# Kernel optimization log

Hardware: AMD Instinct MI355X
Metric: run time of the kernel (lower is better)

## Reference

```python
import jax, jax.numpy as jnp
import numpy as np

NUM_CLASSES = 10
ALPHA = 0.25
GAMMA = 2.0
BETA = 1.0
EPS = 1e-7


def _corners(centers, dims, yaws):
    # centers [N,2], dims [N,2] (l,w), yaws [N] -> corners [N,4,2]
    half = dims * 0.5
    base = jnp.array([[1., 1.], [-1., 1.], [-1., -1.], [1., -1.]], dtype=centers.dtype)
    base = base[None, :, :] * half[:, None, :]  # [N,4,2]
    c, s = jnp.cos(yaws), jnp.sin(yaws)
    x = base[..., 0] * c[:, None] - base[..., 1] * s[:, None]
    y = base[..., 0] * s[:, None] + base[..., 1] * c[:, None]
    corners = jnp.stack([x, y], axis=-1) + centers[:, None, :]
    return corners[:, jnp.array([3, 2, 1, 0]), :]  # reorder as in torch code


def _cross(u, v):
    return u[..., 0] * v[..., 1] - u[..., 1] * v[..., 0]


def _signed_area(q):  # q [...,4,2]
    return 0.5 * jnp.sum(_cross(q, jnp.roll(q, -1, axis=-2)), axis=-1)


def _pts_in_quad(pts, quad, sgn):
    # pts [N,P,2] inside convex quad [N,4,2]; sgn = orientation sign of quad [N]
    a = quad
    e = jnp.roll(quad, -1, axis=-2) - a  # [N,4,2]
    d = pts[:, :, None, :] - a[:, None, :, :]  # [N,P,4,2]
    cr = e[:, None, :, 0] * d[..., 1] - e[:, None, :, 1] * d[..., 0]  # [N,P,4]
    return jnp.all(cr * sgn[:, None, None] >= -1e-9, axis=-1)


def _rotated_iou(cA, cB):
    # Exact convex-quad intersection IoU (replaces the per-box Shapely loop).
    N = cA.shape[0]
    sgnA = jnp.sign(_signed_area(cA))
    sgnB = jnp.sign(_signed_area(cB))
    vA_in_B = _pts_in_quad(cA, cB, sgnB)  # [N,4]
    vB_in_A = _pts_in_quad(cB, cA, sgnA)  # [N,4]
    # all 4x4 edge-edge intersections
    a1 = cA; a2 = jnp.roll(cA, -1, axis=1)
    b1 = cB; b2 = jnp.roll(cB, -1, axis=1)
    da = (a2 - a1)[:, :, None, :]  # [N,4,1,2]
    db = (b2 - b1)[:, None, :, :]  # [N,1,4,2]
    dp = b1[:, None, :, :] - a1[:, :, None, :]  # [N,4,4,2]
    den = _cross(da, db)  # [N,4,4]
    den_safe = jnp.where(jnp.abs(den) < 1e-12, 1.0, den)
    t = _cross(dp, db) / den_safe
    s = _cross(dp, da) / den_safe
    val_x = (jnp.abs(den) > 1e-12) & (t >= 0) & (t <= 1) & (s >= 0) & (s <= 1)
    xpts = a1[:, :, None, :] + t[..., None] * da  # [N,4,4,2]
    # up to 24 candidate vertices of the convex intersection polygon
    pts = jnp.concatenate([cA, cB, xpts.reshape(N, 16, 2)], axis=1)  # [N,24,2]
    valid = jnp.concatenate([vA_in_B, vB_in_A, val_x.reshape(N, 16)], axis=1)
    pts = jnp.where(valid[..., None], pts, 0.0)
    nv = valid.sum(axis=1)
    cent = pts.sum(axis=1) / jnp.maximum(nv, 1)[:, None]
    ang = jnp.arctan2(pts[..., 1] - cent[:, None, 1], pts[..., 0] - cent[:, None, 0])
    key = jnp.where(valid, ang, 1e9)
    order = jnp.argsort(key, axis=1)
    ps = jnp.take_along_axis(pts, order[..., None], axis=1)
    vs = jnp.take_along_axis(valid, order, axis=1)
    ps = jnp.where(vs[..., None], ps, ps[:, :1, :])  # pad with first valid vertex
    inter = 0.5 * jnp.abs(jnp.sum(_cross(ps, jnp.roll(ps, -1, axis=1)), axis=1))
    inter = jnp.where(nv >= 3, inter, 0.0)
    areaA = jnp.abs(_signed_area(cA))
    areaB = jnp.abs(_signed_area(cB))
    union = areaA + areaB - inter
    return jnp.where(union > 1e-7, inter / union, 0.0)


def _sl1(p, t):
    d = jnp.abs(p - t)
    return jnp.where(d < BETA, 0.5 * d * d / BETA, d - 0.5 * BETA)


def setup_inputs() -> dict:
    key = jax.random.key(0)
    ks = jax.random.split(key, 7)
    B, C, H, W = 8, NUM_CLASSES, 256, 256
    cls_pred = jax.random.normal(ks[0], (B, C, H, W), dtype=jnp.float32)
    reg_pred = jax.random.uniform(ks[1], (B, 9, H, W), dtype=jnp.float32)
    iou_pred = jax.random.normal(ks[2], (B, 1, H, W), dtype=jnp.float32)
    cls_targets = jax.random.randint(ks[3], (B, H, W), 0, C, dtype=jnp.int32)
    reg_targets = jax.random.uniform(ks[4], (B, 9, H, W), dtype=jnp.float32)
    reg_weights = jax.random.randint(ks[5], (B, H, W), 0, 2).astype(jnp.float32)
    iou_targets = jax.random.uniform(ks[6], (B, 1, H, W), dtype=jnp.float32)
    return {"cls_pred": cls_pred, "reg_pred": reg_pred, "iou_pred": iou_pred,
            "cls_targets": cls_targets, "reg_targets": reg_targets,
            "reg_weights": reg_weights, "iou_targets": iou_targets}


def reference(cls_pred, reg_pred, iou_pred, cls_targets, reg_targets, reg_weights, iou_targets):
    B, C, H, W = cls_pred.shape
    N = B * H * W
    clsf = jnp.transpose(cls_pred, (0, 2, 3, 1)).reshape(N, C)
    regf = jnp.transpose(reg_pred, (0, 2, 3, 1)).reshape(N, 9)
    regt = jnp.transpose(reg_targets, (0, 2, 3, 1)).reshape(N, 9)
    iouf = jnp.transpose(iou_pred, (0, 2, 3, 1)).reshape(N)
    iout = iou_targets.reshape(N)
    ct = cls_targets.reshape(N)
    w = reg_weights.reshape(N)
    pos = (w > 0).astype(clsf.dtype)
    num_pos = jnp.maximum(pos.sum(), 1.0)
    # focal classification loss
    valid = ct >= 0
    p = jax.nn.softmax(clsf, axis=1)
    tl = jnp.clip(ct, 0, C - 1)
    pt = jnp.clip(jnp.take_along_axis(p, tl[:, None], axis=1)[:, 0], EPS, 1.0 - EPS)
    alpha_t = jnp.where(ct > 0, ALPHA, 1.0 - ALPHA)
    fl = -alpha_t * (1.0 - pt) ** GAMMA * jnp.log(pt)
    cls_loss = jnp.sum(jnp.where(valid, fl, 0.0)) / num_pos
    cen_p, dim_p, yaw_p = regf[:, :2], regf[:, 3:5], regf[:, 6]
    cen_t, dim_t, yaw_t = regt[:, :2], regt[:, 3:5], regt[:, 6]
    cp = _corners(cen_p, dim_p, yaw_p)
    ctg = _corners(cen_t, dim_t, yaw_t)
    iou = jax.lax.stop_gradient(_rotated_iou(cp, ctg))
    d2 = jnp.sum((cen_p - cen_t) ** 2, axis=-1)
    allc = jnp.concatenate([cp, ctg], axis=1)  # [N,8,2]
    c2 = jnp.maximum(jnp.sum((allc.max(axis=1) - allc.min(axis=1)) ** 2, axis=-1), EPS)
    loss_bev = 1.0 - iou + d2 / c2
    at_p = jnp.arctan(dim_p[:, 1] / jnp.maximum(dim_p[:, 0], EPS))
    at_t = jnp.arctan(dim_t[:, 1] / jnp.maximum(dim_t[:, 0], EPS))
    v = (4.0 / np.pi ** 2) * (at_p - at_t) ** 2
    alpha_c = jax.lax.stop_gradient(v / (1.0 - iou + v + EPS))
    loss_bev = loss_bev + alpha_c * v
    bev_loss = jnp.sum(loss_bev * pos) / num_pos
    # smooth-L1 terms: z (ch 2), h (ch 5), vel (ch 7:9)
    z_loss = jnp.sum(_sl1(regf[:, 2], regt[:, 2]) * pos) / num_pos
    h_loss = jnp.sum(_sl1(regf[:, 5], regt[:, 5]) * pos) / num_pos
    vel_loss = jnp.sum(_sl1(regf[:, 7:9], regt[:, 7:9]).sum(axis=-1) * pos) / num_pos
    # BCE-with-logits IoU head loss
    x, y = iouf, iout
    bce = jnp.maximum(x, 0.0) - x * y + jnp.log1p(jnp.exp(-jnp.abs(x)))
    iou_loss = jnp.sum(bce * pos) / num_pos
    return jnp.stack([cls_loss, bev_loss, z_loss, h_loss, vel_loss, iou_loss])
```

## Files before the change

kernel.cpp:

```cpp
#include <hip/hip_runtime.h>
#include <cstdint>
#include <cstddef>

#define B_ 8
#define C_ 10
#define HW_ 65536
#define NPIX_ (B_ * HW_)

__device__ __forceinline__ float sl1f(float p, float t) {
    float d = fabsf(p - t);
    return (d < 1.0f) ? 0.5f * d * d : d - 0.5f;
}

__device__ __forceinline__ void pixel_loss(
    const float lg[C_], int ct, const float P[9], const float T[9],
    float w, float xiou, float yiou, float o[7])
{
    float m = lg[0];
    #pragma unroll
    for (int c = 1; c < C_; c++) m = fmaxf(m, lg[c]);
    float se = 0.f;
    float ex[C_];
    #pragma unroll
    for (int c = 0; c < C_; c++) { ex[c] = __expf(lg[c] - m); se += ex[c]; }
    int tl = ct < 0 ? 0 : (ct > C_ - 1 ? C_ - 1 : ct);
    float et = 0.f;
    #pragma unroll
    for (int c = 0; c < C_; c++) et = (c == tl) ? ex[c] : et;
    float pt = __fdividef(et, se);
    pt = fminf(fmaxf(pt, 1e-7f), 1.0f - 1e-7f);
    float alpha_t = (ct > 0) ? 0.25f : 0.75f;
    float omp = 1.0f - pt;
    float fl = -alpha_t * omp * omp * __logf(pt);
    o[0] = (ct >= 0) ? fl : 0.0f;

    float pos = (w > 0.f) ? 1.f : 0.f;

    float Ax[4], Ay[4], Bx[4], By[4];
    {
        const float sbx[4] = { 1.f, -1.f, -1.f, 1.f };
        const float sby[4] = { -1.f, -1.f, 1.f, 1.f };
        float hx = 0.5f * P[3], hy = 0.5f * P[4];
        float ss, cc; __sincosf(P[6], &ss, &cc);
        #pragma unroll
        for (int i = 0; i < 4; i++) {
            float px = sbx[i] * hx, py = sby[i] * hy;
            Ax[i] = px * cc - py * ss + P[0];
            Ay[i] = px * ss + py * cc + P[1];
        }
        float hx2 = 0.5f * T[3], hy2 = 0.5f * T[4];
        float ss2, cc2; __sincosf(T[6], &ss2, &cc2);
        #pragma unroll
        for (int i = 0; i < 4; i++) {
            float px = sbx[i] * hx2, py = sby[i] * hy2;
            Bx[i] = px * cc2 - py * ss2 + T[0];
            By[i] = px * ss2 + py * cc2 + T[1];
        }
    }

    float sa = 0.f, sb = 0.f;
    #pragma unroll
    for (int i = 0; i < 4; i++) {
        int j = (i + 1) & 3;
        sa += Ax[i] * Ay[j] - Ay[i] * Ax[j];
        sb += Bx[i] * By[j] - By[i] * Bx[j];
    }
    sa *= 0.5f; sb *= 0.5f;
    float sgnA = (sa > 0.f) ? 1.f : ((sa < 0.f) ? -1.f : 0.f);
    float sgnB = (sb > 0.f) ? 1.f : ((sb < 0.f) ? -1.f : 0.f);

    float dB[4][4], dA[4][4];
    #pragma unroll
    for (int j = 0; j < 4; j++) {
        int j1 = (j + 1) & 3;
        float ex_ = Bx[j1] - Bx[j], ey_ = By[j1] - By[j];
        #pragma unroll
        for (int i = 0; i < 4; i++)
            dB[j][i] = sgnB * (ex_ * (Ay[i] - By[j]) - ey_ * (Ax[i] - Bx[j]));
    }
    #pragma unroll
    for (int j = 0; j < 4; j++) {
        int j1 = (j + 1) & 3;
        float ex_ = Ax[j1] - Ax[j], ey_ = Ay[j1] - Ay[j];
        #pragma unroll
        for (int i = 0; i < 4; i++)
            dA[j][i] = sgnA * (ex_ * (By[i] - Ay[j]) - ey_ * (Bx[i] - Ax[j]));
    }

    float S = 0.f;
    #pragma unroll
    for (int i = 0; i < 4; i++) {
        int i1 = (i + 1) & 3;
        float t0 = 0.f, t1 = 1.f;
        #pragma unroll
        for (int j = 0; j < 4; j++) {
            float d0 = dB[j][i], d1 = dB[j][i1];
            float den = d1 - d0;
            float t = __fdividef(-d0, den);
            if (den > 0.f)       t0 = fmaxf(t0, t);
            else if (den < 0.f)  t1 = fminf(t1, t);
            else if (d0 < 0.f)   t0 = 2.f;
        }
        S += (Ax[i] * Ay[i1] - Ay[i] * Ax[i1]) * fmaxf(t1 - t0, 0.f);
    }
    #pragma unroll
    for (int i = 0; i < 4; i++) {
        int i1 = (i + 1) & 3;
        float t0 = 0.f, t1 = 1.f;
        #pragma unroll
        for (int j = 0; j < 4; j++) {
            float d0 = dA[j][i], d1 = dA[j][i1];
            float den = d1 - d0;
            float t = __fdividef(-d0, den);
            if (den > 0.f)       t0 = fmaxf(t0, t);
            else if (den < 0.f)  t1 = fminf(t1, t);
            else if (d0 < 0.f)   t0 = 2.f;
        }
        S += (Bx[i] * By[i1] - By[i] * Bx[i1]) * fmaxf(t1 - t0, 0.f);
    }
    float inter = 0.5f * fabsf(S);

    float areaA = fabsf(sa), areaB = fabsf(sb);
    float uni = areaA + areaB - inter;
    float iou = (uni > 1e-7f) ? __fdividef(inter, uni) : 0.f;

    float ddx = P[0] - T[0], ddy = P[1] - T[1];
    float d2 = ddx * ddx + ddy * ddy;
    float mnx = Ax[0], mxx = Ax[0], mny = Ay[0], mxy = Ay[0];
    #pragma unroll
    for (int i = 1; i < 4; i++) {
        mnx = fminf(mnx, Ax[i]); mxx = fmaxf(mxx, Ax[i]);
        mny = fminf(mny, Ay[i]); mxy = fmaxf(mxy, Ay[i]);
    }
    #pragma unroll
    for (int i = 0; i < 4; i++) {
        mnx = fminf(mnx, Bx[i]); mxx = fmaxf(mxx, Bx[i]);
        mny = fminf(mny, By[i]); mxy = fmaxf(mxy, By[i]);
    }
    float exd = mxx - mnx, eyd = mxy - mny;
    float c2 = fmaxf(exd * exd + eyd * eyd, 1e-7f);

    float atp = atanf(__fdividef(P[4], fmaxf(P[3], 1e-7f)));
    float att = atanf(__fdividef(T[4], fmaxf(T[3], 1e-7f)));
    float dv = atp - att;
    float v = 0.4052847345693511f * dv * dv;
    float alpha_c = __fdividef(v, 1.0f - iou + v + 1e-7f);
    float lbev = 1.0f - iou + __fdividef(d2, c2) + alpha_c * v;
    o[1] = lbev * pos;

    o[2] = sl1f(P[2], T[2]) * pos;
    o[3] = sl1f(P[5], T[5]) * pos;
    o[4] = (sl1f(P[7], T[7]) + sl1f(P[8], T[8])) * pos;

    float bce = fmaxf(xiou, 0.f) - xiou * yiou + __logf(1.0f + __expf(-fabsf(xiou)));
    o[5] = bce * pos;
    o[6] = pos;
}

__global__ __launch_bounds__(256) void bev_loss_main(
    const float* __restrict__ cls_pred, const float* __restrict__ reg_pred,
    const float* __restrict__ iou_pred, const int* __restrict__ cls_tg,
    const float* __restrict__ reg_tg, const float* __restrict__ reg_w,
    const float* __restrict__ iou_tg, double* __restrict__ part)
{
    int t  = blockIdx.x * blockDim.x + threadIdx.x;
    int n0 = t << 1;
    int b  = n0 >> 16;
    int hw = n0 & 65535;

    float2 lg2[C_];
    {
        const float* cp = cls_pred + (size_t)b * C_ * HW_ + hw;
        #pragma unroll
        for (int c = 0; c < C_; c++)
            lg2[c] = *reinterpret_cast<const float2*>(cp + (size_t)c * HW_);
    }
    float2 P2[9], T2[9];
    {
        const float* rp = reg_pred + (size_t)b * 9 * HW_ + hw;
        const float* rt = reg_tg  + (size_t)b * 9 * HW_ + hw;
        #pragma unroll
        for (int k = 0; k < 9; k++) {
            P2[k] = *reinterpret_cast<const float2*>(rp + (size_t)k * HW_);
            T2[k] = *reinterpret_cast<const float2*>(rt + (size_t)k * HW_);
        }
    }
    int2   ct2 = *reinterpret_cast<const int2*>(cls_tg + n0);
    float2 w2  = *reinterpret_cast<const float2*>(reg_w + n0);
    float2 x2  = *reinterpret_cast<const float2*>(iou_pred + n0);
    float2 y2  = *reinterpret_cast<const float2*>(iou_tg + n0);

    float o0[7], o1[7];
    {
        float lg[C_], P[9], T[9];
        #pragma unroll
        for (int c = 0; c < C_; c++) lg[c] = lg2[c].x;
        #pragma unroll
        for (int k = 0; k < 9; k++) { P[k] = P2[k].x; T[k] = T2[k].x; }
        pixel_loss(lg, ct2.x, P, T, w2.x, x2.x, y2.x, o0);
    }
    {
        float lg[C_], P[9], T[9];
        #pragma unroll
        for (int c = 0; c < C_; c++) lg[c] = lg2[c].y;
        #pragma unroll
        for (int k = 0; k < 9; k++) { P[k] = P2[k].y; T[k] = T2[k].y; }
        pixel_loss(lg, ct2.y, P, T, w2.y, x2.y, y2.y, o1);
    }

    __shared__ double red[4][7];
    int lane = threadIdx.x & 63;
    int wv   = threadIdx.x >> 6;
    #pragma unroll
    for (int k = 0; k < 7; k++) {
        double s = (double)o0[k] + (double)o1[k];
        for (int off = 32; off > 0; off >>= 1) s += __shfl_down(s, off, 64);
        if (lane == 0) red[wv][k] = s;
    }
    __syncthreads();
    if (threadIdx.x == 0) {
        #pragma unroll
        for (int k = 0; k < 7; k++)
            part[(size_t)blockIdx.x * 7 + k] = red[0][k] + red[1][k] + red[2][k] + red[3][k];
    }
}

__global__ void bev_loss_fin(const double* __restrict__ part, float* __restrict__ out, int nb) {
    int l = threadIdx.x;
    double s[7] = { 0, 0, 0, 0, 0, 0, 0 };
    for (int i = l; i < nb; i += 64) {
        #pragma unroll
        for (int k = 0; k < 7; k++) s[k] += part[(size_t)i * 7 + k];
    }
    #pragma unroll
    for (int k = 0; k < 7; k++) {
        for (int off = 32; off > 0; off >>= 1) s[k] += __shfl_down(s[k], off, 64);
    }
    if (l == 0) {
        double npos = fmax(s[6], 1.0);
        #pragma unroll
        for (int k = 0; k < 6; k++) out[k] = (float)(s[k] / npos);
    }
}

extern "C" void kernel_launch(void* const* d_in, const int* in_sizes, int n_in,
                              void* d_out, int out_size, void* d_ws, size_t ws_size,
                              hipStream_t stream) {
    const float* cls_pred = (const float*)d_in[0];
    const float* reg_pred = (const float*)d_in[1];
    const float* iou_pred = (const float*)d_in[2];
    const int*   cls_tg   = (const int*)d_in[3];
    const float* reg_tg   = (const float*)d_in[4];
    const float* reg_w    = (const float*)d_in[5];
    const float* iou_tg   = (const float*)d_in[6];
    float* out = (float*)d_out;
    double* part = (double*)d_ws;

    const int nb = 1024;
    bev_loss_main<<<nb, 256, 0, stream>>>(cls_pred, reg_pred, iou_pred, cls_tg,
                                          reg_tg, reg_w, iou_tg, part);
    bev_loss_fin<<<1, 64, 0, stream>>>(part, out, nb);
}
```

Measured before the change: 37.77 us.

## Fuse final reduction into main kernel via atomic ticket and vectorize pixel math as float2

Replaces the separate finalize kernel with a last-block-done pattern: each block writes its partial sums, increments an atomic ticket, and the last block reduces all partials and writes the outputs. The per-pixel loss is rewritten to process two pixels as float2 lanes with branchless selects in the clipping loop, and launch bounds now request 3 waves per SIMD. It adds a memset launch for the ticket and a threadfence per block, trading the second kernel launch for extra synchronisation.

New measurement: 122.4 us. 3.24x slower.

```diff
diff --git a/kernel.cpp b/kernel.cpp
--- a/kernel.cpp
+++ b/kernel.cpp
@@ -6,240 +6,284 @@
 #define C_ 10
 #define HW_ 65536
 #define NPIX_ (B_ * HW_)
-
-__device__ __forceinline__ float sl1f(float p, float t) {
-    float d = fabsf(p - t);
-    return (d < 1.0f) ? 0.5f * d * d : d - 0.5f;
-}
-
-__device__ __forceinline__ void pixel_loss(
-    const float lg[C_], int ct, const float P[9], const float T[9],
-    float w, float xiou, float yiou, float o[7])
-{
-    float m = lg[0];
-    #pragma unroll
-    for (int c = 1; c < C_; c++) m = fmaxf(m, lg[c]);
-    float se = 0.f;
-    float ex[C_];
-    #pragma unroll
-    for (int c = 0; c < C_; c++) { ex[c] = __expf(lg[c] - m); se += ex[c]; }
-    int tl = ct < 0 ? 0 : (ct > C_ - 1 ? C_ - 1 : ct);
-    float et = 0.f;
-    #pragma unroll
-    for (int c = 0; c < C_; c++) et = (c == tl) ? ex[c] : et;
-    float pt = __fdividef(et, se);
-    pt = fminf(fmaxf(pt, 1e-7f), 1.0f - 1e-7f);
-    float alpha_t = (ct > 0) ? 0.25f : 0.75f;
-    float omp = 1.0f - pt;
-    float fl = -alpha_t * omp * omp * __logf(pt);
-    o[0] = (ct >= 0) ? fl : 0.0f;
-
-    float pos = (w > 0.f) ? 1.f : 0.f;
-
-    float Ax[4], Ay[4], Bx[4], By[4];
-    {
-        const float sbx[4] = { 1.f, -1.f, -1.f, 1.f };
-        const float sby[4] = { -1.f, -1.f, 1.f, 1.f };
-        float hx = 0.5f * P[3], hy = 0.5f * P[4];
-        float ss, cc; __sincosf(P[6], &ss, &cc);
-        #pragma unroll
-        for (int i = 0; i < 4; i++) {
-            float px = sbx[i] * hx, py = sby[i] * hy;
-            Ax[i] = px * cc - py * ss + P[0];
-            Ay[i] = px * ss + py * cc + P[1];
-        }
-        float hx2 = 0.5f * T[3], hy2 = 0.5f * T[4];
-        float ss2, cc2; __sincosf(T[6], &ss2, &cc2);
-        #pragma unroll
-        for (int i = 0; i < 4; i++) {
-            float px = sbx[i] * hx2, py = sby[i] * hy2;
-            Bx[i] = px * cc2 - py * ss2 + T[0];
-            By[i] = px * ss2 + py * cc2 + T[1];
-        }
-    }
-
-    float sa = 0.f, sb = 0.f;
-    #pragma unroll
-    for (int i = 0; i < 4; i++) {
-        int j = (i + 1) & 3;
-        sa += Ax[i] * Ay[j] - Ay[i] * Ax[j];
-        sb += Bx[i] * By[j] - By[i] * Bx[j];
-    }
-    sa *= 0.5f; sb *= 0.5f;
-    float sgnA = (sa > 0.f) ? 1.f : ((sa < 0.f) ? -1.f : 0.f);
-    float sgnB = (sb > 0.f) ? 1.f : ((sb < 0.f) ? -1.f : 0.f);
-
-    float dB[4][4], dA[4][4];
-    #pragma unroll
-    for (int j = 0; j < 4; j++) {
-        int j1 = (j + 1) & 3;
-        float ex_ = Bx[j1] - Bx[j], ey_ = By[j1] - By[j];
-        #pragma unroll
-        for (int i = 0; i < 4; i++)
-            dB[j][i] = sgnB * (ex_ * (Ay[i] - By[j]) - ey_ * (Ax[i] - Bx[j]));
-    }
-    #pragma unroll
-    for (int j = 0; j < 4; j++) {
-        int j1 = (j + 1) & 3;
-        float ex_ = Ax[j1] - Ax[j], ey_ = Ay[j1] - Ay[j];
-        #pragma unroll
-        for (int i = 0; i < 4; i++)
-            dA[j][i] = sgnA * (ex_ * (By[i] - Ay[j]) - ey_ * (Bx[i] - Ax[j]));
-    }
-
-    float S = 0.f;
-    #pragma unroll
-    for (int i = 0; i < 4; i++) {
-        int i1 = (i + 1) & 3;
-        float t0 = 0.f, t1 = 1.f;
-        #pragma unroll
-        for (int j = 0; j < 4; j++) {
-            float d0 = dB[j][i], d1 = dB[j][i1];
-            float den = d1 - d0;
-            float t = __fdividef(-d0, den);
-            if (den > 0.f)       t0 = fmaxf(t0, t);
-            else if (den < 0.f)  t1 = fminf(t1, t);
-            else if (d0 < 0.f)   t0 = 2.f;
-        }
-        S += (Ax[i] * Ay[i1] - Ay[i] * Ax[i1]) * fmaxf(t1 - t0, 0.f);
-    }
-    #pragma unroll
-    for (int i = 0; i < 4; i++) {
-        int i1 = (i + 1) & 3;
-        float t0 = 0.f, t1 = 1.f;
-        #pragma unroll
-        for (int j = 0; j < 4; j++) {
-            float d0 = dA[j][i], d1 = dA[j][i1];
-            float den = d1 - d0;
-            float t = __fdividef(-d0, den);
-            if (den > 0.f)       t0 = fmaxf(t0, t);
-            else if (den < 0.f)  t1 = fminf(t1, t);
-            else if (d0 < 0.f)   t0 = 2.f;
-        }
-        S += (Bx[i] * By[i1] - By[i] * Bx[i1]) * fmaxf(t1 - t0, 0.f);
-    }
-    float inter = 0.5f * fabsf(S);
-
-    float areaA = fabsf(sa), areaB = fabsf(sb);
-    float uni = areaA + areaB - inter;
-    float iou = (uni > 1e-7f) ? __fdividef(inter, uni) : 0.f;
-
-    float ddx = P[0] - T[0], ddy = P[1] - T[1];
-    float d2 = ddx * ddx + ddy * ddy;
-    float mnx = Ax[0], mxx = Ax[0], mny = Ay[0], mxy = Ay[0];
-    #pragma unroll
-    for (int i = 1; i < 4; i++) {
-        mnx = fminf(mnx, Ax[i]); mxx = fmaxf(mxx, Ax[i]);
-        mny = fminf(mny, Ay[i]); mxy = fmaxf(mxy, Ay[i]);
-    }
-    #pragma unroll
-    for (int i = 0; i < 4; i++) {
-        mnx = fminf(mnx, Bx[i]); mxx = fmaxf(mxx, Bx[i]);
-        mny = fminf(mny, By[i]); mxy = fmaxf(mxy, By[i]);
-    }
-    float exd = mxx - mnx, eyd = mxy - mny;
-    float c2 = fmaxf(exd * exd + eyd * eyd, 1e-7f);
-
-    float atp = atanf(__fdividef(P[4], fmaxf(P[3], 1e-7f)));
-    float att = atanf(__fdividef(T[4], fmaxf(T[3], 1e-7f)));
-    float dv = atp - att;
-    float v = 0.4052847345693511f * dv * dv;
-    float alpha_c = __fdividef(v, 1.0f - iou + v + 1e-7f);
-    float lbev = 1.0f - iou + __fdividef(d2, c2) + alpha_c * v;
-    o[1] = lbev * pos;
-
-    o[2] = sl1f(P[2], T[2]) * pos;
-    o[3] = sl1f(P[5], T[5]) * pos;
-    o[4] = (sl1f(P[7], T[7]) + sl1f(P[8], T[8])) * pos;
-
-    float bce = fmaxf(xiou, 0.f) - xiou * yiou + __logf(1.0f + __expf(-fabsf(xiou)));
-    o[5] = bce * pos;
-    o[6] = pos;
-}
-
-__global__ __launch_bounds__(256) void bev_loss_main(
+#define NB_ 1024
+
+__device__ __forceinline__ float2 mk2(float a, float b) { float2 r; r.x = a; r.y = b; return r; }
+__device__ __forceinline__ float2 bc2(float a) { return mk2(a, a); }
+__device__ __forceinline__ float2 add2(float2 a, float2 b) { return mk2(a.x + b.x, a.y + b.y); }
+__device__ __forceinline__ float2 sub2(float2 a, float2 b) { return mk2(a.x - b.x, a.y - b.y); }
+__device__ __forceinline__ float2 mul2(float2 a, float2 b) { return mk2(a.x * b.x, a.y * b.y); }
+__device__ __forceinline__ float2 fma2(float2 a, float2 b, float2 c) {
+    return mk2(fmaf(a.x, b.x, c.x), fmaf(a.y, b.y, c.y));
+}
+__device__ __forceinline__ float2 max2(float2 a, float2 b) { return mk2(fmaxf(a.x, b.x), fmaxf(a.y, b.y)); }
+__device__ __forceinline__ float2 min2(float2 a, float2 b) { return mk2(fminf(a.x, b.x), fminf(a.y, b.y)); }
+__device__ __forceinline__ float2 abs2(float2 a) { return mk2(fabsf(a.x), fabsf(a.y)); }
+__device__ __forceinline__ float2 neg2(float2 a) { return mk2(-a.x, -a.y); }
+__device__ __forceinline__ float2 div2(float2 a, float2 b) {
+    return mk2(__fdividef(a.x, b.x), __fdividef(a.y, b.y));
+}
+__device__ __forceinline__ float2 expf2(float2 a) { return mk2(__expf(a.x), __expf(a.y)); }
+__device__ __forceinline__ float2 logf2(float2 a) { return mk2(__logf(a.x), __logf(a.y)); }
+__device__ __forceinline__ float sgnf(float v) { return (v > 0.f) ? 1.f : ((v < 0.f) ? -1.f : 0.f); }
+__device__ __forceinline__ float2 sl12(float2 p, float2 t) {
+    float2 d = abs2(sub2(p, t));
+    float rx = (d.x < 1.f) ? 0.5f * d.x * d.x : d.x - 0.5f;
+    float ry = (d.y < 1.f) ? 0.5f * d.y * d.y : d.y - 0.5f;
+    return mk2(rx, ry);
+}
+
+__global__ __launch_bounds__(256, 3) void bev_loss_main(
     const float* __restrict__ cls_pred, const float* __restrict__ reg_pred,
     const float* __restrict__ iou_pred, const int* __restrict__ cls_tg,
     const float* __restrict__ reg_tg, const float* __restrict__ reg_w,
-    const float* __restrict__ iou_tg, double* __restrict__ part)
+    const float* __restrict__ iou_tg, double* __restrict__ part,
+    unsigned int* __restrict__ ticket, float* __restrict__ out)
 {
     int t  = blockIdx.x * blockDim.x + threadIdx.x;
     int n0 = t << 1;
     int b  = n0 >> 16;
     int hw = n0 & 65535;
 
-    float2 lg2[C_];
+    float2 lg[C_];
     {
         const float* cp = cls_pred + (size_t)b * C_ * HW_ + hw;
         #pragma unroll
         for (int c = 0; c < C_; c++)
-            lg2[c] = *reinterpret_cast<const float2*>(cp + (size_t)c * HW_);
-    }
-    float2 P2[9], T2[9];
+            lg[c] = *reinterpret_cast<const float2*>(cp + (size_t)c * HW_);
+    }
+    float2 P[9], T[9];
     {
         const float* rp = reg_pred + (size_t)b * 9 * HW_ + hw;
         const float* rt = reg_tg  + (size_t)b * 9 * HW_ + hw;
         #pragma unroll
         for (int k = 0; k < 9; k++) {
-            P2[k] = *reinterpret_cast<const float2*>(rp + (size_t)k * HW_);
-            T2[k] = *reinterpret_cast<const float2*>(rt + (size_t)k * HW_);
+            P[k] = *reinterpret_cast<const float2*>(rp + (size_t)k * HW_);
+            T[k] = *reinterpret_cast<const float2*>(rt + (size_t)k * HW_);
         }
     }
     int2   ct2 = *reinterpret_cast<const int2*>(cls_tg + n0);
     float2 w2  = *reinterpret_cast<const float2*>(reg_w + n0);
-    float2 x2  = *reinterpret_cast<const float2*>(iou_pred + n0);
-    float2 y2  = *reinterpret_cast<const float2*>(iou_tg + n0);
-
-    float o0[7], o1[7];
-    {
-        float lg[C_], P[9], T[9];
-        #pragma unroll
-        for (int c = 0; c < C_; c++) lg[c] = lg2[c].x;
-        #pragma unroll
-        for (int k = 0; k < 9; k++) { P[k] = P2[k].x; T[k] = T2[k].x; }
-        pixel_loss(lg, ct2.x, P, T, w2.x, x2.x, y2.x, o0);
-    }
-    {
-        float lg[C_], P[9], T[9];
-        #pragma unroll
-        for (int c = 0; c < C_; c++) lg[c] = lg2[c].y;
-        #pragma unroll
-        for (int k = 0; k < 9; k++) { P[k] = P2[k].y; T[k] = T2[k].y; }
-        pixel_loss(lg, ct2.y, P, T, w2.y, x2.y, y2.y, o1);
-    }
-
-    __shared__ double red[4][7];
+    float2 xi  = *reinterpret_cast<const float2*>(iou_pred + n0);
+    float2 yi  = *reinterpret_cast<const float2*>(iou_tg + n0);
+
+    float2 o0;
+    {
+        float2 m = lg[0];
+        #pragma unroll
+        for (int c = 1; c < C_; c++) m = max2(m, lg[c]);
+        int tlx = ct2.x < 0 ? 0 : (ct2.x > C_ - 1 ? C_ - 1 : ct2.x);
+        int tly = ct2.y < 0 ? 0 : (ct2.y > C_ - 1 ? C_ - 1 : ct2.y);
+        float2 se = bc2(0.f), et = bc2(0.f);
+        #pragma unroll
+        for (int c = 0; c < C_; c++) {
+            float2 e = expf2(sub2(lg[c], m));
+            se = add2(se, e);
+            et.x = (c == tlx) ? e.x : et.x;
+            et.y = (c == tly) ? e.y : et.y;
+        }
+        float2 pt = div2(et, se);
+        pt = min2(max2(pt, bc2(1e-7f)), bc2(1.0f - 1e-7f));
+        float2 at = mk2(ct2.x > 0 ? 0.25f : 0.75f, ct2.y > 0 ? 0.25f : 0.75f);
+        float2 omp = sub2(bc2(1.f), pt);
+        float2 fl = mul2(neg2(at), mul2(mul2(omp, omp), logf2(pt)));
+        o0 = mk2(ct2.x >= 0 ? fl.x : 0.f, ct2.y >= 0 ? fl.y : 0.f);
+    }
+
+    float2 pos = mk2(w2.x > 0.f ? 1.f : 0.f, w2.y > 0.f ? 1.f : 0.f);
+
+    float2 Ax[4], Ay[4], Bx[4], By[4];
+    {
+        const float sbx[4] = { 1.f, -1.f, -1.f, 1.f };
+        const float sby[4] = { -1.f, -1.f, 1.f, 1.f };
+        float ssx, ccx, ssy, ccy;
+        __sincosf(P[6].x, &ssx, &ccx); __sincosf(P[6].y, &ssy, &ccy);
+        float2 ss = mk2(ssx, ssy), cc = mk2(ccx, ccy);
+        float2 hx = mul2(bc2(0.5f), P[3]), hy = mul2(bc2(0.5f), P[4]);
+        #pragma unroll
+        for (int i = 0; i < 4; i++) {
+            float2 px = mul2(bc2(sbx[i]), hx), py = mul2(bc2(sby[i]), hy);
+            Ax[i] = add2(sub2(mul2(px, cc), mul2(py, ss)), P[0]);
+            Ay[i] = add2(fma2(px, ss, mul2(py, cc)), P[1]);
+        }
+        __sincosf(T[6].x, &ssx, &ccx); __sincosf(T[6].y, &ssy, &ccy);
+        ss = mk2(ssx, ssy); cc = mk2(ccx, ccy);
+        hx = mul2(bc2(0.5f), T[3]); hy = mul2(bc2(0.5f), T[4]);
+        #pragma unroll
+        for (int i = 0; i < 4; i++) {
+            float2 px = mul2(bc2(sbx[i]), hx), py = mul2(bc2(sby[i]), hy);
+            Bx[i] = add2(sub2(mul2(px, cc), mul2(py, ss)), T[0]);
+            By[i] = add2(fma2(px, ss, mul2(py, cc)), T[1]);
+        }
+    }
+
+    float2 sa = bc2(0.f), sb = bc2(0.f);
+    #pragma unroll
+    for (int i = 0; i < 4; i++) {
+        int j = (i + 1) & 3;
+        sa = add2(sa, sub2(mul2(Ax[i], Ay[j]), mul2(Ay[i], Ax[j])));
+        sb = add2(sb, sub2(mul2(Bx[i], By[j]), mul2(By[i], Bx[j])));
+    }
+    sa = mul2(bc2(0.5f), sa); sb = mul2(bc2(0.5f), sb);
+    float2 sgnA = mk2(sgnf(sa.x), sgnf(sa.y));
+    float2 sgnB = mk2(sgnf(sb.x), sgnf(sb.y));
+
+    float2 S = bc2(0.f);
+    {
+        float2 dB[4][4];
+        #pragma unroll
+        for (int j = 0; j < 4; j++) {
+            int j1 = (j + 1) & 3;
+            float2 sx = mul2(sgnB, sub2(Bx[j1], Bx[j]));
+            float2 sy = mul2(sgnB, sub2(By[j1], By[j]));
+            float2 kj = sub2(mul2(sx, By[j]), mul2(sy, Bx[j]));
+            #pragma unroll
+            for (int i = 0; i < 4; i++)
+                dB[j][i] = sub2(sub2(mul2(sx, Ay[i]), mul2(sy, Ax[i])), kj);
+        }
+        #pragma unroll
+        for (int i = 0; i < 4; i++) {
+            int i1 = (i + 1) & 3;
+            float2 t0 = bc2(0.f), t1 = bc2(1.f);
+            #pragma unroll
+            for (int j = 0; j < 4; j++) {
+                float2 d0 = dB[j][i], d1 = dB[j][i1];
+                float2 den = sub2(d1, d0);
+                float2 tt = div2(neg2(d0), den);
+                float e0x = (den.x > 0.f) ? tt.x : ((den.x == 0.f && d0.x < 0.f) ? 2.f : 0.f);
+                float e0y = (den.y > 0.f) ? tt.y : ((den.y == 0.f && d0.y < 0.f) ? 2.f : 0.f);
+                t0 = max2(t0, mk2(e0x, e0y));
+                float e1x = (den.x < 0.f) ? tt.x : 1.f;
+                float e1y = (den.y < 0.f) ? tt.y : 1.f;
+                t1 = min2(t1, mk2(e1x, e1y));
+            }
+            float2 cr = sub2(mul2(Ax[i], Ay[i1]), mul2(Ay[i], Ax[i1]));
+            S = add2(S, mul2(cr, max2(sub2(t1, t0), bc2(0.f))));
+        }
+    }
+    {
+        float2 dA[4][4];
+        #pragma unroll
+        for (int j = 0; j < 4; j++) {
+            int j1 = (j + 1) & 3;
+            float2 sx = mul2(sgnA, sub2(Ax[j1], Ax[j]));
+            float2 sy = mul2(sgnA, sub2(Ay[j1], Ay[j]));
+            float2 kj = sub2(mul2(sx, Ay[j]), mul2(sy, Ax[j]));
+            #pragma unroll
+            for (int i = 0; i < 4; i++)
+                dA[j][i] = sub2(sub2(mul2(sx, By[i]), mul2(sy, Bx[i])), kj);
+        }
+        #pragma unroll
+        for (int i = 0; i < 4; i++) {
+            int i1 = (i + 1) & 3;
+            float2 t0 = bc2(0.f), t1 = bc2(1.f);
+            #pragma unroll
+            for (int j = 0; j < 4; j++) {
+                float2 d0 = dA[j][i], d1 = dA[j][i1];
+                float2 den = sub2(d1, d0);
+                float2 tt = div2(neg2(d0), den);
+                float e0x = (den.x > 0.f) ? tt.x : ((den.x == 0.f && d0.x < 0.f) ? 2.f : 0.f);
+                float e0y = (den.y > 0.f) ? tt.y : ((den.y == 0.f && d0.y < 0.f) ? 2.f : 0.f);
+                t0 = max2(t0, mk2(e0x, e0y));
+                float e1x = (den.x < 0.f) ? tt.x : 1.f;
+                float e1y = (den.y < 0.f) ? tt.y : 1.f;
+                t1 = min2(t1, mk2(e1x, e1y));
+            }
+            float2 cr = sub2(mul2(Bx[i], By[i1]), mul2(By[i], Bx[i1]));
+            S = add2(S, mul2(cr, max2(sub2(t1, t0), bc2(0.f))));
+        }
+    }
+    float2 inter = mul2(bc2(0.5f), abs2(S));
+    float2 areaA = abs2(sa), areaB = abs2(sb);
+    float2 uni = sub2(add2(areaA, areaB), inter);
+    float2 iou;
+    iou.x = (uni.x > 1e-7f) ? __fdividef(inter.x, uni.x) : 0.f;
+    iou.y = (uni.y > 1e-7f) ? __fdividef(inter.y, uni.y) : 0.f;
+
+    float2 o1;
+    {
+        float2 ddx = sub2(P[0], T[0]), ddy = sub2(P[1], T[1]);
+        float2 d2v = fma2(ddx, ddx, mul2(ddy, ddy));
+        float2 mnx = Ax[0], mxx = Ax[0], mny = Ay[0], mxy = Ay[0];
+        #pragma unroll
+        for (int i = 1; i < 4; i++) {
+            mnx = min2(mnx, Ax[i]); mxx = max2(mxx, Ax[i]);
+            mny = min2(mny, Ay[i]); mxy = max2(mxy, Ay[i]);
+        }
+        #pragma unroll
+        for (int i = 0; i < 4; i++) {
+            mnx = min2(mnx, Bx[i]); mxx = max2(mxx, Bx[i]);
+            mny = min2(mny, By[i]); mxy = max2(mxy, By[i]);
+        }
+        float2 exd = sub2(mxx, mnx), eyd = sub2(mxy, mny);
+        float2 c2v = max2(fma2(exd, exd, mul2(eyd, eyd)), bc2(1e-7f));
+        float2 atp = mk2(atanf(__fdividef(P[4].x, fmaxf(P[3].x, 1e-7f))),
+                         atanf(__fdividef(P[4].y, fmaxf(P[3].y, 1e-7f))));
+        float2 att = mk2(atanf(__fdividef(T[4].x, fmaxf(T[3].x, 1e-7f))),
+                         atanf(__fdividef(T[4].y, fmaxf(T[3].y, 1e-7f))));
+        float2 dv = sub2(atp, att);
+        float2 vv = mul2(bc2(0.4052847345693511f), mul2(dv, dv));
+        float2 dn = add2(add2(sub2(bc2(1.f), iou), vv), bc2(1e-7f));
+        float2 alpha_c = div2(vv, dn);
+        float2 lbev = add2(add2(sub2(bc2(1.f), iou), div2(d2v, c2v)), mul2(alpha_c, vv));
+        o1 = mul2(lbev, pos);
+    }
+
+    float2 o2 = mul2(sl12(P[2], T[2]), pos);
+    float2 o3 = mul2(sl12(P[5], T[5]), pos);
+    float2 o4 = mul2(add2(sl12(P[7], T[7]), sl12(P[8], T[8])), pos);
+    float2 bce = add2(sub2(max2(xi, bc2(0.f)), mul2(xi, yi)),
+                      logf2(add2(bc2(1.f), expf2(neg2(abs2(xi))))));
+    float2 o5 = mul2(bce, pos);
+
+    double a[7] = {
+        (double)o0.x + (double)o0.y, (double)o1.x + (double)o1.y,
+        (double)o2.x + (double)o2.y, (double)o3.x + (double)o3.y,
+        (double)o4.x + (double)o4.y, (double)o5.x + (double)o5.y,
+        (double)pos.x + (double)pos.y
+    };
+    __shared__ double red[7][4];
+    __shared__ bool lastf;
     int lane = threadIdx.x & 63;
     int wv   = threadIdx.x >> 6;
     #pragma unroll
     for (int k = 0; k < 7; k++) {
-        double s = (double)o0[k] + (double)o1[k];
+        double s = a[k];
         for (int off = 32; off > 0; off >>= 1) s += __shfl_down(s, off, 64);
-        if (lane == 0) red[wv][k] = s;
+        if (lane == 0) red[k][wv] = s;
     }
     __syncthreads();
     if (threadIdx.x == 0) {
         #pragma unroll
         for (int k = 0; k < 7; k++)
-            part[(size_t)blockIdx.x * 7 + k] = red[0][k] + red[1][k] + red[2][k] + red[3][k];
-    }
-}
-
-__global__ void bev_loss_fin(const double* __restrict__ part, float* __restrict__ out, int nb) {
-    int l = threadIdx.x;
+            part[(size_t)k * NB_ + blockIdx.x] = red[k][0] + red[k][1] + red[k][2] + red[k][3];
+    }
+    __threadfence();
+    if (threadIdx.x == 0) {
+        unsigned tk = atomicAdd(ticket, 1u);
+        lastf = (tk == NB_ - 1);
+    }
+    __syncthreads();
+    if (!lastf) return;
+
+    __threadfence();
     double s[7] = { 0, 0, 0, 0, 0, 0, 0 };
-    for (int i = l; i < nb; i += 64) {
-        #pragma unroll
-        for (int k = 0; k < 7; k++) s[k] += part[(size_t)i * 7 + k];
-    }
+    #pragma unroll
+    for (int k = 0; k < 7; k++)
+        for (int r = threadIdx.x; r < NB_; r += 256)
+            s[k] += part[(size_t)k * NB_ + r];
     #pragma unroll
     for (int k = 0; k < 7; k++) {
-        for (int off = 32; off > 0; off >>= 1) s[k] += __shfl_down(s[k], off, 64);
-    }
-    if (l == 0) {
-        double npos = fmax(s[6], 1.0);
-        #pragma unroll
-        for (int k = 0; k < 6; k++) out[k] = (float)(s[k] / npos);
+        double v = s[k];
+        for (int off = 32; off > 0; off >>= 1) v += __shfl_down(v, off, 64);
+        if (lane == 0) red[k][wv] = v;
+    }
+    __syncthreads();
+    if (threadIdx.x == 0) {
+        double npos = fmax(red[6][0] + red[6][1] + red[6][2] + red[6][3], 1.0);
+        #pragma unroll
+        for (int k = 0; k < 6; k++)
+            out[k] = (float)((red[k][0] + red[k][1] + red[k][2] + red[k][3]) / npos);
     }
 }
 
@@ -254,10 +298,12 @@
     const float* reg_w    = (const float*)d_in[5];
     const float* iou_tg   = (const float*)d_in[6];
     float* out = (float*)d_out;
+
     double* part = (double*)d_ws;
-
-    const int nb = 1024;
-    bev_loss_main<<<nb, 256, 0, stream>>>(cls_pred, reg_pred, iou_pred, cls_tg,
-                                          reg_tg, reg_w, iou_tg, part);
-    bev_loss_fin<<<1, 64, 0, stream>>>(part, out, nb);
-}
+    unsigned int* ticket = (unsigned int*)((char*)d_ws + (size_t)7 * NB_ * sizeof(double));
+
+    hipMemsetAsync(ticket, 0, sizeof(unsigned int), stream);
+
+    bev_loss_main<<<NB_, 256, 0, stream>>>(cls_pred, reg_pred, iou_pred, cls_tg,
+                                           reg_tg, reg_w, iou_tg, part, ticket, out);
+}
```
